# Kernel optimization log

Hardware: AMD Instinct MI355X
Metric: run time of the kernel (lower is better)

The kernel has to match this reference:

```python
import jax, jax.numpy as jnp
import numpy as np

B, T, C = 4, 2048, 1024
NUM_HEADS, HEAD_DIM = 16, 64
INNER = NUM_HEADS * HEAD_DIM
OUT_DIM = 1024


def setup_inputs() -> dict:
    key = jax.random.key(0)
    kx, kk, kq, kv, kp = jax.random.split(key, 5)
    return {
        "x": jax.random.normal(kx, (B, T, C), dtype=jnp.float32),
        "W_k": jax.random.normal(kk, (INNER, C), dtype=jnp.float32),
        "W_q": jax.random.normal(kq, (INNER, C), dtype=jnp.float32),
        "W_v": jax.random.normal(kv, (INNER, C), dtype=jnp.float32),
        "W_p": jax.random.normal(kp, (OUT_DIM, INNER), dtype=jnp.float32),
    }


def reference(x, W_k, W_q, W_v, W_p):
    b, t, c = x.shape
    h, d = NUM_HEADS, HEAD_DIM
    scale_in = c ** (-0.5)
    # project and split heads: [B, H, T, D]
    def proj(W):
        y = jnp.einsum('btc,ic->bti', x, W) * scale_in
        return y.reshape(b, t, h, d).transpose(0, 2, 1, 3)
    k = proj(W_k)
    q = proj(W_q)
    v = proj(W_v)
    scores = jnp.einsum('bhqd,bhkd->bhqk', q, k) * (d ** (-0.5))
    weight = jax.nn.softmax(scores, axis=-1)
    out = jnp.einsum('bhqk,bhkd->bhqd', weight, v)  # [B,H,T,D]
    out = out.transpose(0, 2, 1, 3).reshape(b, t, h * d)
    out = jnp.einsum('bti,oi->bto', out, W_p) * (W_p.shape[-1] ** (-0.5))
    return out
```

## Files before the change

kernel.cpp:

```cpp
#include <hip/hip_runtime.h>
#include <math.h>

typedef __attribute__((ext_vector_type(8))) short bh8;
typedef __attribute__((ext_vector_type(4))) float f32x4;
typedef __attribute__((ext_vector_type(2))) unsigned u32x2;

namespace {
constexpr int Bn = 4, Tn = 2048, Cn = 1024, Hn = 16, Dn = 64, INNERn = 1024, OUTn = 1024;
constexpr int Mn = Bn * Tn;
}

__device__ __forceinline__ void glds16(const void* g, void* l) {
    __builtin_amdgcn_global_load_lds(
        (const __attribute__((address_space(1))) void*)g,
        (__attribute__((address_space(3))) void*)l, 16, 0, 0);
}

__device__ __forceinline__ void barrier_vm0() {
    __builtin_amdgcn_s_waitcnt(0x0070);
    __builtin_amdgcn_s_barrier();
}

__device__ __forceinline__ ushort f2bf(float f) {
    union { float f; unsigned u; } v; v.f = f;
    unsigned r = v.u + 0x7fffu + ((v.u >> 16) & 1u);
    return (ushort)(r >> 16);
}
__device__ __forceinline__ unsigned pack_rne(float a, float b) {
    return (unsigned)f2bf(a) | ((unsigned)f2bf(b) << 16);
}
__device__ __forceinline__ unsigned pack_trunc(float a, float b) {
    return __builtin_amdgcn_perm(__float_as_uint(a), __float_as_uint(b), 0x03020706u);
}

__global__ __launch_bounds__(256)
void cvt_all(const float* __restrict__ x,  const float* __restrict__ Wk,
             const float* __restrict__ Wq, const float* __restrict__ Wv,
             const float* __restrict__ Wp,
             ushort* __restrict__ xb,  ushort* __restrict__ wkb,
             ushort* __restrict__ wqb, ushort* __restrict__ wvb,
             ushort* __restrict__ wpb)
{
    const int bid = blockIdx.x;
    const float* s; ushort* d; float sc; int i;
    if (bid < 8192) {
        s = x; d = xb; sc = 0.03125f;
        i = bid * 256 + threadIdx.x;
    } else {
        const int seg = (bid - 8192) >> 10;
        i = ((bid - 8192) & 1023) * 256 + threadIdx.x;
        s  = (seg == 0) ? Wk : (seg == 1) ? Wq : (seg == 2) ? Wv : Wp;
        d  = (seg == 0) ? wkb : (seg == 1) ? wqb : (seg == 2) ? wvb : wpb;
        sc = (seg == 3) ? 0.03125f : 1.0f;
    }
    float4 f = ((const float4*)s)[i];
    ushort4 o;
    o.x = f2bf(f.x * sc); o.y = f2bf(f.y * sc);
    o.z = f2bf(f.z * sc); o.w = f2bf(f.w * sc);
    ((ushort4*)d)[i] = o;
}

__global__ __launch_bounds__(256)
void gemm_qkv(const ushort* __restrict__ A, const ushort* __restrict__ Wq,
              const ushort* __restrict__ Wk, const ushort* __restrict__ Wv,
              ushort* __restrict__ Oq, ushort* __restrict__ Ok,
              ushort* __restrict__ Ovt, float qscale)
{
    __shared__ char SM[32768];
    char* As0 = SM;          char* As1 = SM + 8192;
    char* Bs0 = SM + 16384;  char* Bs1 = SM + 24576;
    const int tid = threadIdx.x;
    const int w = tid >> 6, lane = tid & 63, quad = lane >> 4, l = lane & 15;
    const int lid = blockIdx.x;
    const int xcd = lid & 7, j = lid >> 3;
    const int ytile = xcd * 8 + j / 24;
    const int xx = j % 24;
    const int sel = xx >> 3;
    const ushort* Bw = (sel == 0) ? Wq : (sel == 1) ? Wk : Wv;
    const int n0 = (xx & 7) * 128, m0 = ytile * 128;
    const int wm = w >> 1, wn = w & 1;

    auto stage = [&](char* Ad, char* Bd, int k0) {
#pragma unroll
        for (int rr = 0; rr < 2; ++rr) {
            const int rho = w * 2 + rr;
            const int row = rho * 16 + (lane >> 2);
            const int kq  = (lane & 3) * 8;
            glds16(A  + (size_t)(m0 + row) * Cn + k0 + kq, Ad + rho * 1024 + lane * 16);
            glds16(Bw + (size_t)(n0 + row) * Cn + k0 + kq, Bd + rho * 1024 + lane * 16);
        }
    };

    f32x4 acc[4][4];
#pragma unroll
    for (int i = 0; i < 4; ++i)
#pragma unroll
        for (int j2 = 0; j2 < 4; ++j2) acc[i][j2] = (f32x4){0.f, 0.f, 0.f, 0.f};

    stage(As0, Bs0, 0);
    barrier_vm0();
#pragma unroll 2
    for (int it = 0; it < 32; ++it) {
        const int cur = it & 1;
        if (it < 31) stage(cur ? As0 : As1, cur ? Bs0 : Bs1, (it + 1) * 32);
        const char* Ac = cur ? As1 : As0; const char* Bc = cur ? Bs1 : Bs0;
        bh8 af[4], bf[4];
#pragma unroll
        for (int mf = 0; mf < 4; ++mf)
            af[mf] = *(const bh8*)(Ac + (wm * 64 + mf * 16 + l) * 64 + quad * 16);
#pragma unroll
        for (int nf = 0; nf < 4; ++nf)
            bf[nf] = *(const bh8*)(Bc + (wn * 64 + nf * 16 + l) * 64 + quad * 16);
#pragma unroll
        for (int mf = 0; mf < 4; ++mf)
#pragma unroll
            for (int nf = 0; nf < 4; ++nf)
                acc[mf][nf] = __builtin_amdgcn_mfma_f32_16x16x32_bf16(af[mf], bf[nf], acc[mf][nf], 0, 0, 0);
        barrier_vm0();
    }

    if (sel < 2) {
        ushort* dU = (sel == 0) ? Oq : Ok;
        const float scale = (sel == 0) ? qscale : 1.0f;
#pragma unroll
        for (int mf = 0; mf < 4; ++mf)
#pragma unroll
            for (int nf = 0; nf < 4; ++nf) {
                const int mb = m0 + wm * 64 + mf * 16 + quad * 4;
                const int n  = n0 + wn * 64 + nf * 16 + l;
                const int h = n >> 6, dd = n & 63;
#pragma unroll
                for (int reg = 0; reg < 4; ++reg) {
                    const int m = mb + reg;
                    const int b = m >> 11, t = m & (Tn - 1);
                    dU[((size_t)(b * Hn + h) * Tn + t) * Dn + dd] = f2bf(acc[mf][nf][reg] * scale);
                }
            }
    } else {
#pragma unroll
        for (int mf = 0; mf < 4; ++mf)
#pragma unroll
            for (int nf = 0; nf < 4; ++nf) {
                const int mb = wm * 64 + mf * 16 + quad * 4;
                const int n  = wn * 64 + nf * 16 + l;
                uint2 p;
                p.x = pack_rne(acc[mf][nf][0], acc[mf][nf][1]);
                p.y = pack_rne(acc[mf][nf][2], acc[mf][nf][3]);
                const int c = mb >> 3;
                *(uint2*)(SM + n * 256 + ((c ^ (n & 15)) & 15) * 16 + (mb & 7) * 2) = p;
            }
        __syncthreads();
        const int bb = m0 >> 11, t0 = m0 & (Tn - 1);
#pragma unroll
        for (int it2 = 0; it2 < 8; ++it2) {
            const int n = it2 * 16 + w * 4 + quad;
            const int ng = n0 + n;
            const int h = ng >> 6, dd = ng & 63;
            int4 vsm = *(const int4*)(SM + n * 256 + ((l ^ (n & 15)) & 15) * 16);
            *(int4*)(Ovt + ((size_t)(bb * Hn + h) * Dn + dd) * Tn + t0 + l * 8) = vsm;
        }
    }
}

__global__ __launch_bounds__(256)
void gemm_po(const ushort* __restrict__ A, const ushort* __restrict__ Bw,
             float* __restrict__ Cout)
{
    __shared__ char As[2][8192];
    __shared__ char Bs[2][8192];
    const int tid = threadIdx.x;
    const int w = tid >> 6, lane = tid & 63, quad = lane >> 4, l = lane & 15;
    const int lid = blockIdx.x;
    const int xcd = lid & 7, j = lid >> 3;
    const int n0 = (j & 7) * 128, m0 = (xcd * 8 + (j >> 3)) * 128;
    const int wm = w >> 1, wn = w & 1;

    auto stage = [&](int bsel, int k0) {
#pragma unroll
        for (int rr = 0; rr < 2; ++rr) {
            const int rho = w * 2 + rr;
            const int row = rho * 16 + (lane >> 2);
            const int kq  = (lane & 3) * 8;
            glds16(A  + (size_t)(m0 + row) * Cn + k0 + kq, As[bsel] + rho * 1024 + lane * 16);
            glds16(Bw + (size_t)(n0 + row) * Cn + k0 + kq, Bs[bsel] + rho * 1024 + lane * 16);
        }
    };

    f32x4 acc[4][4];
#pragma unroll
    for (int i = 0; i < 4; ++i)
#pragma unroll
        for (int j2 = 0; j2 < 4; ++j2) acc[i][j2] = (f32x4){0.f, 0.f, 0.f, 0.f};

    stage(0, 0);
    barrier_vm0();
#pragma unroll 2
    for (int it = 0; it < 32; ++it) {
        const int cur = it & 1;
        if (it < 31) stage(cur ^ 1, (it + 1) * 32);
        const char* Ac = As[cur]; const char* Bc = Bs[cur];
        bh8 af[4], bf[4];
#pragma unroll
        for (int mf = 0; mf < 4; ++mf)
            af[mf] = *(const bh8*)(Ac + (wm * 64 + mf * 16 + l) * 64 + quad * 16);
#pragma unroll
        for (int nf = 0; nf < 4; ++nf)
            bf[nf] = *(const bh8*)(Bc + (wn * 64 + nf * 16 + l) * 64 + quad * 16);
#pragma unroll
        for (int mf = 0; mf < 4; ++mf)
#pragma unroll
            for (int nf = 0; nf < 4; ++nf)
                acc[mf][nf] = __builtin_amdgcn_mfma_f32_16x16x32_bf16(af[mf], bf[nf], acc[mf][nf], 0, 0, 0);
        barrier_vm0();
    }

#pragma unroll
    for (int mf = 0; mf < 4; ++mf)
#pragma unroll
        for (int nf = 0; nf < 4; ++nf) {
            const int mb = m0 + wm * 64 + mf * 16 + quad * 4;
            const int n  = n0 + wn * 64 + nf * 16 + l;
#pragma unroll
            for (int reg = 0; reg < 4; ++reg)
                Cout[(size_t)(mb + reg) * OUTn + n] = acc[mf][nf][reg];
        }
}

__global__ __launch_bounds__(256, 4)
void attn_mfma(const ushort* __restrict__ Qg, const ushort* __restrict__ Kg,
               const ushort* __restrict__ Vtg, ushort* __restrict__ Og)
{
    __shared__ char KT[2][8192];
    __shared__ char VT[2][8192];

    const int tid = threadIdx.x;
    const int w = tid >> 6, lane = tid & 63, quad = lane >> 4, l = lane & 15;
    const int lid = blockIdx.x;
    const int xcd = lid & 7, j = lid >> 3;
    const int bh = (xcd << 3) | (j >> 4);
    const int q0 = (j & 15) * 128;
    const int b = bh >> 4, h = bh & 15;
    const ushort* Qp = Qg  + (size_t)bh * Tn * Dn;
    const ushort* Kp = Kg  + (size_t)bh * Tn * Dn;
    const ushort* Vp = Vtg + (size_t)bh * Dn * Tn;

    auto stageK = [&](char* buf, int kt) {
#pragma unroll
        for (int rr = 0; rr < 2; ++rr) {
            const int rho = w * 2 + rr;
            const int r8  = lane >> 3;
            const int r   = rho * 8 + r8;
            const int dc  = (lane & 7) ^ r8;
            glds16(Kp + (size_t)(kt * 64 + r) * Dn + dc * 8, buf + rho * 1024 + lane * 16);
        }
    };
    auto stageV = [&](char* buf, int kt) {
#pragma unroll
        for (int rr = 0; rr < 2; ++rr) {
            const int rho = w * 2 + rr;
            const int d = rho * 8 + (lane >> 3);
            const int csrc = (lane & 7) ^ ((lane >> 3) & 7);
            glds16(Vp + (size_t)d * Tn + kt * 64 + csrc * 8, buf + rho * 1024 + lane * 16);
        }
    };

    bh8 qf[2][2];
#pragma unroll
    for (int nt = 0; nt < 2; ++nt)
#pragma unroll
        for (int ks = 0; ks < 2; ++ks)
            qf[nt][ks] = *(const bh8*)(Qp + (size_t)(q0 + w * 32 + nt * 16 + l) * Dn + ks * 32 + quad * 8);

    bh8 ones;
#pragma unroll
    for (int i = 0; i < 8; ++i) ones[i] = (short)0x3F80;

    f32x4 oacc[2][4], lacc[2];
#pragma unroll
    for (int nt = 0; nt < 2; ++nt) {
        lacc[nt] = (f32x4){0.f, 0.f, 0.f, 0.f};
#pragma unroll
        for (int dt = 0; dt < 4; ++dt) oacc[nt][dt] = (f32x4){0.f, 0.f, 0.f, 0.f};
    }

    const f32x4 zero = (f32x4){0.f, 0.f, 0.f, 0.f};

    stageK(KT[0], 0);
    stageV(VT[0], 0);
    barrier_vm0();

#pragma unroll 2
    for (int kt = 0; kt < Tn / 64; ++kt) {
        const int cur = kt & 1;
        if (kt < Tn / 64 - 1) {
            stageK(KT[cur ^ 1], kt + 1);
            stageV(VT[cur ^ 1], kt + 1);
        }
        const char* Kc = KT[cur];
        const char* Vc = VT[cur];

#pragma unroll
        for (int hh = 0; hh < 2; ++hh) {
            bh8 kf[2][2];
#pragma unroll
            for (int k8l = 0; k8l < 2; ++k8l) {
                const int row = (hh * 2 + k8l) * 16 + l;
#pragma unroll
                for (int ks = 0; ks < 2; ++ks)
                    kf[k8l][ks] = *(const bh8*)(Kc + row * 128 + (((ks * 4 + quad) ^ (l & 7)) * 16));
            }

            f32x4 st[2][2];
            __builtin_amdgcn_s_setprio(1);
#pragma unroll
            for (int nt = 0; nt < 2; ++nt)
#pragma unroll
                for (int k8l = 0; k8l < 2; ++k8l) {
                    st[nt][k8l] = __builtin_amdgcn_mfma_f32_16x16x32_bf16(kf[k8l][0], qf[nt][0], zero, 0, 0, 0);
                    st[nt][k8l] = __builtin_amdgcn_mfma_f32_16x16x32_bf16(kf[k8l][1], qf[nt][1], st[nt][k8l], 0, 0, 0);
                }
            __builtin_amdgcn_s_setprio(0);

            bh8 pf[2];
#pragma unroll
            for (int nt = 0; nt < 2; ++nt) {
                const unsigned a0 = pack_trunc(__builtin_amdgcn_exp2f(st[nt][0][0]),
                                               __builtin_amdgcn_exp2f(st[nt][0][1]));
                const unsigned a1 = pack_trunc(__builtin_amdgcn_exp2f(st[nt][0][2]),
                                               __builtin_amdgcn_exp2f(st[nt][0][3]));
                const unsigned b0 = pack_trunc(__builtin_amdgcn_exp2f(st[nt][1][0]),
                                               __builtin_amdgcn_exp2f(st[nt][1][1]));
                const unsigned b1 = pack_trunc(__builtin_amdgcn_exp2f(st[nt][1][2]),
                                               __builtin_amdgcn_exp2f(st[nt][1][3]));
                const u32x2 p = __builtin_amdgcn_permlane32_swap(a0, b0, false, false);
                const u32x2 q = __builtin_amdgcn_permlane16_swap(p.x, p.y, false, false);
                const u32x2 r = __builtin_amdgcn_permlane32_swap(a1, b1, false, false);
                const u32x2 s = __builtin_amdgcn_permlane16_swap(r.x, r.y, false, false);
                union { unsigned u[4]; bh8 v; } pu;
                pu.u[0] = q.x; pu.u[1] = s.x; pu.u[2] = q.y; pu.u[3] = s.y;
                pf[nt] = pu.v;
            }

            bh8 vf[4];
#pragma unroll
            for (int dt = 0; dt < 4; ++dt)
                vf[dt] = *(const bh8*)(Vc + (dt * 16 + l) * 128 + (((hh * 4 + quad) ^ (l & 7)) * 16));
            __builtin_amdgcn_s_setprio(1);
#pragma unroll
            for (int nt = 0; nt < 2; ++nt)
                lacc[nt] = __builtin_amdgcn_mfma_f32_16x16x32_bf16(ones, pf[nt], lacc[nt], 0, 0, 0);
#pragma unroll
            for (int dt = 0; dt < 4; ++dt)
#pragma unroll
                for (int nt = 0; nt < 2; ++nt)
                    oacc[nt][dt] = __builtin_amdgcn_mfma_f32_16x16x32_bf16(vf[dt], pf[nt], oacc[nt][dt], 0, 0, 0);
            __builtin_amdgcn_s_setprio(0);
        }
        barrier_vm0();
    }

#pragma unroll
    for (int nt = 0; nt < 2; ++nt) {
        const float inv = 1.0f / lacc[nt][0];
        const int t = q0 + w * 32 + nt * 16 + l;
#pragma unroll
        for (int dt = 0; dt < 4; ++dt) {
            uint2 p;
            p.x = pack_rne(oacc[nt][dt][0] * inv, oacc[nt][dt][1] * inv);
            p.y = pack_rne(oacc[nt][dt][2] * inv, oacc[nt][dt][3] * inv);
            *(uint2*)(Og + ((size_t)(b * Tn + t)) * INNERn + h * 64 + dt * 16 + quad * 4) = p;
        }
    }
}

extern "C" void kernel_launch(void* const* d_in, const int* in_sizes, int n_in,
                              void* d_out, int out_size, void* d_ws, size_t ws_size,
                              hipStream_t stream)
{
    const float* x  = (const float*)d_in[0];
    const float* Wk = (const float*)d_in[1];
    const float* Wq = (const float*)d_in[2];
    const float* Wv = (const float*)d_in[3];
    const float* Wp = (const float*)d_in[4];
    float* out = (float*)d_out;

    ushort* xb  = (ushort*)d_ws;
    ushort* wkb = xb  + (size_t)Mn * Cn;
    ushort* wqb = wkb + (size_t)INNERn * Cn;
    ushort* wvb = wqb + (size_t)INNERn * Cn;
    ushort* wpb = wvb + (size_t)INNERn * Cn;
    ushort* qw  = wpb + (size_t)OUTn * INNERn;
    ushort* kw  = qw  + (size_t)Mn * INNERn;
    ushort* vtw = kw  + (size_t)Mn * INNERn;
    ushort* aow = vtw + (size_t)Mn * INNERn;

    const dim3 blk(256);
    cvt_all<<<dim3(8192 + 4096), blk, 0, stream>>>(x, Wk, Wq, Wv, Wp,
                                                   xb, wkb, wqb, wvb, wpb);

    gemm_qkv<<<dim3(1536), blk, 0, stream>>>(xb, wqb, wkb, wvb,
                                             qw, kw, vtw, 0.125f * 1.44269504f);

    attn_mfma<<<dim3(1024), blk, 0, stream>>>(qw, kw, vtw, aow);

    gemm_po<<<dim3(512), blk, 0, stream>>>(aow, wpb, out);
}
```

Before: 256.7 us.

## Rewrite QKV GEMM with 256x256 tiles, 8 waves and split-phase pipelining

The QKV projection GEMM moves from 128x128 tiles with 4 waves to 256x256 tiles with 8 waves (512 threads), using a 64KB double-buffered LDS with XOR-swizzled layout. Each k-step is split into two MFMA halves, with A and B loads for the next steps interleaved between them and s_setprio raised around the MFMA blocks. The V-transpose epilogue is done in four quadrant passes through LDS. Larger tiles raise arithmetic intensity and cut global traffic, but the grid drops to 384 blocks, which may underfill the CUs, and the manual waitcnt and barrier scheduling adds correctness risk.

```diff
diff --git a/kernel.cpp b/kernel.cpp
--- a/kernel.cpp
+++ b/kernel.cpp
@@ -60,73 +60,117 @@
     ((ushort4*)d)[i] = o;
 }
 
-__global__ __launch_bounds__(256)
+__device__ __forceinline__ void gemm256_core(const ushort* __restrict__ A,
+                                             const ushort* __restrict__ Bw,
+                                             const int m0, const int n0,
+                                             char* LDS_, f32x4 (&acc)[8][4])
+{
+    const int tid = threadIdx.x;
+    const int w = tid >> 6, lane = tid & 63, quad = lane >> 4, l = lane & 15;
+    const int wm = w >> 2, wn = w & 3;
+
+    auto stageHalf = [&](int isB, int dbuf, int half, int rowg0, int kt) {
+        char* base = LDS_ + isB * 32768 + dbuf * 16384 + half * 8192;
+        const ushort* G = isB ? Bw : A;
+        const int row = tid >> 2, slot = tid & 3;
+        glds16(G + (size_t)(rowg0 + half * 128 + row) * Cn + kt * 32
+                 + ((slot ^ ((tid >> 3) & 3)) * 8),
+               base + tid * 16);
+    };
+    auto ldA = [&](int dbuf, int mf) -> bh8 {
+        return *(const bh8*)(LDS_ + dbuf * 16384 + wm * 8192
+                             + (mf * 16 + l) * 64
+                             + ((quad ^ ((l >> 1) & 3)) * 16));
+    };
+    auto ldB = [&](int dbuf, int nf) -> bh8 {
+        return *(const bh8*)(LDS_ + 32768 + dbuf * 16384 + (wn >> 1) * 8192
+                             + ((wn & 1) * 64 + nf * 16 + l) * 64
+                             + ((quad ^ ((l >> 1) & 3)) * 16));
+    };
+
+    stageHalf(1, 0, 0, n0, 0); stageHalf(1, 0, 1, n0, 0);
+    stageHalf(0, 0, 0, m0, 0); stageHalf(0, 0, 1, m0, 0);
+    stageHalf(1, 1, 0, n0, 1); stageHalf(1, 1, 1, n0, 1);
+    __builtin_amdgcn_s_waitcnt(0x0F72);
+    __builtin_amdgcn_s_barrier();
+
+#pragma unroll 2
+    for (int t = 0; t < 32; ++t) {
+        const int d = t & 1;
+        bh8 af[4], bf[4], ag[4];
+#pragma unroll
+        for (int mf = 0; mf < 4; ++mf) af[mf] = ldA(d, mf);
+#pragma unroll
+        for (int nf = 0; nf < 4; ++nf) bf[nf] = ldB(d, nf);
+        if (t + 1 < 32) {
+            stageHalf(0, (t + 1) & 1, 0, m0, t + 1);
+            stageHalf(0, (t + 1) & 1, 1, m0, t + 1);
+        }
+        __builtin_amdgcn_s_barrier();
+        __builtin_amdgcn_s_waitcnt(0xC07F);
+        __builtin_amdgcn_s_setprio(1);
+#pragma unroll
+        for (int mf = 0; mf < 4; ++mf)
+#pragma unroll
+            for (int nf = 0; nf < 4; ++nf)
+                acc[mf][nf] = __builtin_amdgcn_mfma_f32_16x16x32_bf16(af[mf], bf[nf], acc[mf][nf], 0, 0, 0);
+        __builtin_amdgcn_s_setprio(0);
+        __builtin_amdgcn_s_barrier();
+#pragma unroll
+        for (int mf = 0; mf < 4; ++mf) ag[mf] = ldA(d, mf + 4);
+        if (t + 2 < 32) {
+            stageHalf(1, d, 0, n0, t + 2);
+            stageHalf(1, d, 1, n0, t + 2);
+        }
+        __builtin_amdgcn_s_barrier();
+        __builtin_amdgcn_s_waitcnt(0xC07F);
+        __builtin_amdgcn_s_setprio(1);
+#pragma unroll
+        for (int mf = 0; mf < 4; ++mf)
+#pragma unroll
+            for (int nf = 0; nf < 4; ++nf)
+                acc[mf + 4][nf] = __builtin_amdgcn_mfma_f32_16x16x32_bf16(ag[mf], bf[nf], acc[mf + 4][nf], 0, 0, 0);
+        __builtin_amdgcn_s_setprio(0);
+        if (t + 2 < 32) __builtin_amdgcn_s_waitcnt(0x0F72);
+        else            __builtin_amdgcn_s_waitcnt(0x0F70);
+        __builtin_amdgcn_s_barrier();
+    }
+}
+
+__global__ __launch_bounds__(512, 2)
 void gemm_qkv(const ushort* __restrict__ A, const ushort* __restrict__ Wq,
               const ushort* __restrict__ Wk, const ushort* __restrict__ Wv,
               ushort* __restrict__ Oq, ushort* __restrict__ Ok,
               ushort* __restrict__ Ovt, float qscale)
 {
-    __shared__ char SM[32768];
-    char* As0 = SM;          char* As1 = SM + 8192;
-    char* Bs0 = SM + 16384;  char* Bs1 = SM + 24576;
+    __shared__ char LDS_[65536];
     const int tid = threadIdx.x;
     const int w = tid >> 6, lane = tid & 63, quad = lane >> 4, l = lane & 15;
+    const int wm = w >> 2, wn = w & 3;
     const int lid = blockIdx.x;
     const int xcd = lid & 7, j = lid >> 3;
-    const int ytile = xcd * 8 + j / 24;
-    const int xx = j % 24;
-    const int sel = xx >> 3;
+    const int mt = xcd * 4 + j / 12;
+    const int rest = j % 12;
+    const int sel = rest >> 2, ntile = rest & 3;
     const ushort* Bw = (sel == 0) ? Wq : (sel == 1) ? Wk : Wv;
-    const int n0 = (xx & 7) * 128, m0 = ytile * 128;
-    const int wm = w >> 1, wn = w & 1;
-
-    auto stage = [&](char* Ad, char* Bd, int k0) {
-#pragma unroll
-        for (int rr = 0; rr < 2; ++rr) {
-            const int rho = w * 2 + rr;
-            const int row = rho * 16 + (lane >> 2);
-            const int kq  = (lane & 3) * 8;
-            glds16(A  + (size_t)(m0 + row) * Cn + k0 + kq, Ad + rho * 1024 + lane * 16);
-            glds16(Bw + (size_t)(n0 + row) * Cn + k0 + kq, Bd + rho * 1024 + lane * 16);
-        }
-    };
-
-    f32x4 acc[4][4];
-#pragma unroll
-    for (int i = 0; i < 4; ++i)
+    const int m0 = mt * 256, n0 = ntile * 256;
+
+    f32x4 acc[8][4];
+#pragma unroll
+    for (int i = 0; i < 8; ++i)
 #pragma unroll
         for (int j2 = 0; j2 < 4; ++j2) acc[i][j2] = (f32x4){0.f, 0.f, 0.f, 0.f};
 
-    stage(As0, Bs0, 0);
-    barrier_vm0();
-#pragma unroll 2
-    for (int it = 0; it < 32; ++it) {
-        const int cur = it & 1;
-        if (it < 31) stage(cur ? As0 : As1, cur ? Bs0 : Bs1, (it + 1) * 32);
-        const char* Ac = cur ? As1 : As0; const char* Bc = cur ? Bs1 : Bs0;
-        bh8 af[4], bf[4];
-#pragma unroll
-        for (int mf = 0; mf < 4; ++mf)
-            af[mf] = *(const bh8*)(Ac + (wm * 64 + mf * 16 + l) * 64 + quad * 16);
-#pragma unroll
-        for (int nf = 0; nf < 4; ++nf)
-            bf[nf] = *(const bh8*)(Bc + (wn * 64 + nf * 16 + l) * 64 + quad * 16);
-#pragma unroll
-        for (int mf = 0; mf < 4; ++mf)
-#pragma unroll
-            for (int nf = 0; nf < 4; ++nf)
-                acc[mf][nf] = __builtin_amdgcn_mfma_f32_16x16x32_bf16(af[mf], bf[nf], acc[mf][nf], 0, 0, 0);
-        barrier_vm0();
-    }
+    gemm256_core(A, Bw, m0, n0, LDS_, acc);
 
     if (sel < 2) {
         ushort* dU = (sel == 0) ? Oq : Ok;
         const float scale = (sel == 0) ? qscale : 1.0f;
 #pragma unroll
-        for (int mf = 0; mf < 4; ++mf)
+        for (int mf = 0; mf < 8; ++mf)
 #pragma unroll
             for (int nf = 0; nf < 4; ++nf) {
-                const int mb = m0 + wm * 64 + mf * 16 + quad * 4;
+                const int mb = m0 + wm * 128 + mf * 16 + quad * 4;
                 const int n  = n0 + wn * 64 + nf * 16 + l;
                 const int h = n >> 6, dd = n & 63;
 #pragma unroll
@@ -138,27 +182,36 @@
             }
     } else {
 #pragma unroll
-        for (int mf = 0; mf < 4; ++mf)
-#pragma unroll
-            for (int nf = 0; nf < 4; ++nf) {
-                const int mb = wm * 64 + mf * 16 + quad * 4;
-                const int n  = wn * 64 + nf * 16 + l;
-                uint2 p;
-                p.x = pack_rne(acc[mf][nf][0], acc[mf][nf][1]);
-                p.y = pack_rne(acc[mf][nf][2], acc[mf][nf][3]);
-                const int c = mb >> 3;
-                *(uint2*)(SM + n * 256 + ((c ^ (n & 15)) & 15) * 16 + (mb & 7) * 2) = p;
+        for (int sm = 0; sm < 2; ++sm)
+#pragma unroll
+            for (int sn = 0; sn < 2; ++sn) {
+                __builtin_amdgcn_s_barrier();
+                if (wm == sm && (wn >> 1) == sn) {
+#pragma unroll
+                    for (int mf = 0; mf < 8; ++mf)
+#pragma unroll
+                        for (int nf = 0; nf < 4; ++nf) {
+                            const int mbL = mf * 16 + quad * 4;
+                            const int nL  = (wn & 1) * 64 + nf * 16 + l;
+                            uint2 p;
+                            p.x = pack_rne(acc[mf][nf][0], acc[mf][nf][1]);
+                            p.y = pack_rne(acc[mf][nf][2], acc[mf][nf][3]);
+                            const int c = mbL >> 3;
+                            *(uint2*)(LDS_ + nL * 256 + ((c ^ (nL & 15)) & 15) * 16 + (mbL & 7) * 2) = p;
+                        }
+                }
+                __builtin_amdgcn_s_waitcnt(0xC07F);
+                __builtin_amdgcn_s_barrier();
+                const int bb = (m0 + sm * 128) >> 11, t0 = (m0 + sm * 128) & (Tn - 1);
+#pragma unroll
+                for (int it2 = 0; it2 < 4; ++it2) {
+                    const int nL = it2 * 32 + w * 4 + quad;
+                    const int ng = n0 + sn * 128 + nL;
+                    const int h = ng >> 6, dd = ng & 63;
+                    int4 vsm = *(const int4*)(LDS_ + nL * 256 + ((l ^ (nL & 15)) & 15) * 16);
+                    *(int4*)(Ovt + ((size_t)(bb * Hn + h) * Dn + dd) * Tn + t0 + l * 8) = vsm;
+                }
             }
-        __syncthreads();
-        const int bb = m0 >> 11, t0 = m0 & (Tn - 1);
-#pragma unroll
-        for (int it2 = 0; it2 < 8; ++it2) {
-            const int n = it2 * 16 + w * 4 + quad;
-            const int ng = n0 + n;
-            const int h = ng >> 6, dd = ng & 63;
-            int4 vsm = *(const int4*)(SM + n * 256 + ((l ^ (n & 15)) & 15) * 16);
-            *(int4*)(Ovt + ((size_t)(bb * Hn + h) * Dn + dd) * Tn + t0 + l * 8) = vsm;
-        }
     }
 }
 
@@ -398,8 +451,8 @@
     cvt_all<<<dim3(8192 + 4096), blk, 0, stream>>>(x, Wk, Wq, Wv, Wp,
                                                    xb, wkb, wqb, wvb, wpb);
 
-    gemm_qkv<<<dim3(1536), blk, 0, stream>>>(xb, wqb, wkb, wvb,
-                                             qw, kw, vtw, 0.125f * 1.44269504f);
+    gemm_qkv<<<dim3(384), dim3(512), 0, stream>>>(xb, wqb, wkb, wvb,
+                                                  qw, kw, vtw, 0.125f * 1.44269504f);
 
     attn_mfma<<<dim3(1024), blk, 0, stream>>>(qw, kw, vtw, aow);
 
```

Result: no change. 254.9 us (-0.7%).

## Load output-projection GEMM operands directly from global into registers, dropping LDS staging

Applied to the files above, without the earlier changes.

The output projection GEMM no longer stages A and B tiles through double-buffered LDS with barriers. Each wave now computes its own 64x64 tile, reading MFMA fragments straight from global memory into registers with a two-stage register prefetch, and raises wave priority around the MFMA bursts. This removes LDS traffic and block-wide barriers. In exchange, operands are no longer shared between waves, so global and L2 traffic per FLOP rises, and the per-lane 16-byte row-strided loads coalesce poorly.

```diff
diff --git a/kernel.cpp b/kernel.cpp
--- a/kernel.cpp
+++ b/kernel.cpp
@@ -166,60 +166,55 @@
 void gemm_po(const ushort* __restrict__ A, const ushort* __restrict__ Bw,
              float* __restrict__ Cout)
 {
-    __shared__ char As[2][8192];
-    __shared__ char Bs[2][8192];
     const int tid = threadIdx.x;
     const int w = tid >> 6, lane = tid & 63, quad = lane >> 4, l = lane & 15;
     const int lid = blockIdx.x;
     const int xcd = lid & 7, j = lid >> 3;
-    const int n0 = (j & 7) * 128, m0 = (xcd * 8 + (j >> 3)) * 128;
-    const int wm = w >> 1, wn = w & 1;
-
-    auto stage = [&](int bsel, int k0) {
-#pragma unroll
-        for (int rr = 0; rr < 2; ++rr) {
-            const int rho = w * 2 + rr;
-            const int row = rho * 16 + (lane >> 2);
-            const int kq  = (lane & 3) * 8;
-            glds16(A  + (size_t)(m0 + row) * Cn + k0 + kq, As[bsel] + rho * 1024 + lane * 16);
-            glds16(Bw + (size_t)(n0 + row) * Cn + k0 + kq, Bs[bsel] + rho * 1024 + lane * 16);
-        }
+    const int mgrp  = (xcd << 2) | (j >> 4);
+    const int ntile = j & 15;
+    const int m0 = (mgrp * 4 + w) * 64;
+    const int n0 = ntile * 64;
+
+    const ushort* Ap = A  + (size_t)(m0 + l) * Cn + quad * 8;
+    const ushort* Bp = Bw + (size_t)(n0 + l) * Cn + quad * 8;
+
+    f32x4 acc[4][4];
+#pragma unroll
+    for (int i = 0; i < 4; ++i)
+#pragma unroll
+        for (int j2 = 0; j2 < 4; ++j2) acc[i][j2] = (f32x4){0.f, 0.f, 0.f, 0.f};
+
+    auto ld = [&](const ushort* P, bh8 (&dst)[4], int it) {
+#pragma unroll
+        for (int f = 0; f < 4; ++f)
+            dst[f] = *(const bh8*)(P + (size_t)f * 16 * Cn + it * 32);
     };
-
-    f32x4 acc[4][4];
-#pragma unroll
-    for (int i = 0; i < 4; ++i)
-#pragma unroll
-        for (int j2 = 0; j2 < 4; ++j2) acc[i][j2] = (f32x4){0.f, 0.f, 0.f, 0.f};
-
-    stage(0, 0);
-    barrier_vm0();
-#pragma unroll 2
-    for (int it = 0; it < 32; ++it) {
-        const int cur = it & 1;
-        if (it < 31) stage(cur ^ 1, (it + 1) * 32);
-        const char* Ac = As[cur]; const char* Bc = Bs[cur];
-        bh8 af[4], bf[4];
-#pragma unroll
-        for (int mf = 0; mf < 4; ++mf)
-            af[mf] = *(const bh8*)(Ac + (wm * 64 + mf * 16 + l) * 64 + quad * 16);
-#pragma unroll
-        for (int nf = 0; nf < 4; ++nf)
-            bf[nf] = *(const bh8*)(Bc + (wn * 64 + nf * 16 + l) * 64 + quad * 16);
+    auto mm = [&](bh8 (&af)[4], bh8 (&bf)[4]) {
+        __builtin_amdgcn_s_setprio(1);
 #pragma unroll
         for (int mf = 0; mf < 4; ++mf)
 #pragma unroll
             for (int nf = 0; nf < 4; ++nf)
                 acc[mf][nf] = __builtin_amdgcn_mfma_f32_16x16x32_bf16(af[mf], bf[nf], acc[mf][nf], 0, 0, 0);
-        barrier_vm0();
+        __builtin_amdgcn_s_setprio(0);
+    };
+
+    bh8 a0[4], b0[4], a1[4], b1[4];
+    ld(Ap, a0, 0); ld(Bp, b0, 0);
+#pragma unroll 2
+    for (int it = 0; it < 32; it += 2) {
+        if (it + 1 < 32) { ld(Ap, a1, it + 1); ld(Bp, b1, it + 1); }
+        mm(a0, b0);
+        if (it + 2 < 32) { ld(Ap, a0, it + 2); ld(Bp, b0, it + 2); }
+        if (it + 1 < 32) mm(a1, b1);
     }
 
 #pragma unroll
     for (int mf = 0; mf < 4; ++mf)
 #pragma unroll
         for (int nf = 0; nf < 4; ++nf) {
-            const int mb = m0 + wm * 64 + mf * 16 + quad * 4;
-            const int n  = n0 + wn * 64 + nf * 16 + l;
+            const int mb = m0 + mf * 16 + quad * 4;
+            const int n  = n0 + nf * 16 + l;
 #pragma unroll
             for (int reg = 0; reg < 4; ++reg)
                 Cout[(size_t)(mb + reg) * OUTn + n] = acc[mf][nf][reg];
```

Result: slower. 304.3 us (+18.5%).
